# Kernel optimization log

Measured on AMD Instinct MI355X. Metric: run time of the kernel, lower is better.

## Reference

```python
import jax, jax.numpy as jnp
import numpy as np

B, N, D = 8, 1024, 768
H = 12
HD = D // H  # 64
SCALE = HD ** -0.5


def setup_inputs() -> dict:
    key = jax.random.key(0)
    k1, k2, k3 = jax.random.split(key, 3)
    x = jax.random.normal(k1, (B, N, D), dtype=jnp.float32)
    qkv_w = jax.random.normal(k2, (3 * D, D), dtype=jnp.float32) * 0.02
    proj_w = jax.random.normal(k3, (D, D), dtype=jnp.float32) * 0.02
    proj_b = jnp.zeros((D,), dtype=jnp.float32)
    return {"x": x, "qkv_w": qkv_w, "proj_w": proj_w, "proj_b": proj_b}


def reference(x, qkv_w, proj_w, proj_b):
    # qkv projection: [B,N,3D] -> [3,B,H,N,HD]
    qkv = jnp.einsum('bnd,ed->bne', x, qkv_w)
    qkv = qkv.reshape(B, N, 3, H, HD).transpose(2, 0, 3, 1, 4)
    q, k, v = qkv[0], qkv[1], qkv[2]
    # scaled dot-product attention
    attn = jnp.einsum('bhqd,bhkd->bhqk', q * SCALE, k)
    attn = jax.nn.softmax(attn, axis=-1)
    out = jnp.einsum('bhqk,bhkd->bhqd', attn, v)
    out = out.transpose(0, 2, 1, 3).reshape(B, N, D)
    # output projection
    return jnp.einsum('bnd,ed->bne', out, proj_w) + proj_b
```

## Files before the change

### kernel.cpp

```cpp
#include <hip/hip_runtime.h>

typedef unsigned short ushort;
typedef __attribute__((ext_vector_type(4)))  float  f32x4;
typedef __attribute__((ext_vector_type(16))) float  f32x16;
typedef __attribute__((ext_vector_type(8)))  short  s16x8;
typedef __attribute__((ext_vector_type(4)))  ushort u16x4;
typedef __attribute__((ext_vector_type(4)))  unsigned u32x4;

#define MFMA16(a, b, c) __builtin_amdgcn_mfma_f32_16x16x32_bf16((a), (b), (c), 0, 0, 0)
#define MFMA32(a, b, c) __builtin_amdgcn_mfma_f32_32x32x16_bf16((a), (b), (c), 0, 0, 0)

__device__ __forceinline__ ushort f2bf(float f) {
    unsigned u = __builtin_bit_cast(unsigned, f);
    u = (u + 0x7FFF + ((u >> 16) & 1)) >> 16;
    return (ushort)u;
}

__device__ __forceinline__ unsigned cvtpk_bf16(float lo, float hi) {
    unsigned r;
    asm("v_cvt_pk_bf16_f32 %0, %1, %2" : "=v"(r) : "v"(lo), "v"(hi));
    return r;
}
__device__ __forceinline__ void plswap(unsigned& a, unsigned& b) {
    asm volatile("v_permlane32_swap_b32 %0, %1" : "+v"(a), "+v"(b));
}
__device__ __forceinline__ float pairmax(float x) {
    return fmaxf(x, __shfl_xor(x, 32));
}
__device__ __forceinline__ float pairsum(float x) {
    return x + __shfl_xor(x, 32);
}
__device__ __forceinline__ float fast_exp2(float x) {
    float r;
    asm("v_exp_f32 %0, %1" : "=v"(r) : "v"(x));
    return r;
}

__device__ __forceinline__ void gload_lds16(const ushort* g, ushort* l) {
    __builtin_amdgcn_global_load_lds(
        (const __attribute__((address_space(1))) void*)g,
        (__attribute__((address_space(3))) void*)l, 16, 0, 0);
}

__global__ __launch_bounds__(256) void cvt_f32_bf16(
    const float* __restrict__ in, ushort* __restrict__ out, int n4)
{
    int i = blockIdx.x * blockDim.x + threadIdx.x;
    const int stride = gridDim.x * blockDim.x;
    for (; i < n4; i += stride) {
        const float4 v = ((const float4*)in)[i];
        u16x4 o;
        o[0] = f2bf(v.x); o[1] = f2bf(v.y); o[2] = f2bf(v.z); o[3] = f2bf(v.w);
        ((u16x4*)out)[i] = o;
    }
}

__device__ __forceinline__ void gemm128_mainloop(
    const ushort* __restrict__ A, const ushort* __restrict__ B, int K,
    int row0, int col0, ushort* As, ushort* Bs, f32x4 acc[4][4])
{
    const int t  = threadIdx.x;
    const int l  = t & 63;
    const int w  = t >> 6;
    const int lr = l & 15, lg = l >> 4;
    const int wm = w >> 1, wn = w & 1;

#pragma unroll
    for (int m = 0; m < 4; m++)
#pragma unroll
        for (int n = 0; n < 4; n++) acc[m][n] = (f32x4){0.f, 0.f, 0.f, 0.f};

    const ushort* ga0 = A + (row0 + (t >> 2)) * K + (t & 3) * 8;
    const ushort* gb0 = B + (col0 + (t >> 2)) * K + (t & 3) * 8;
    const int rowsz = 64 * K;
    ushort* la0 = As + t * 8;
    ushort* lb0 = Bs + t * 8;

    auto STAGE = [&](int kt, int buf) {
        const int k0  = kt * 32;
        const int off = buf * 4096;
        gload_lds16(ga0 + k0,         la0 + off);
        gload_lds16(ga0 + rowsz + k0, la0 + off + 2048);
        gload_lds16(gb0 + k0,         lb0 + off);
        gload_lds16(gb0 + rowsz + k0, lb0 + off + 2048);
    };
    auto COMPUTE = [&](int buf) {
        const ushort* Ab = As + buf * 4096;
        const ushort* Bb = Bs + buf * 4096;
        s16x8 af[4], bfr[4];
#pragma unroll
        for (int m = 0; m < 4; m++)
            af[m] = *(const s16x8*)&Ab[(wm * 64 + m * 16 + lr) * 32 + lg * 8];
#pragma unroll
        for (int n = 0; n < 4; n++)
            bfr[n] = *(const s16x8*)&Bb[(wn * 64 + n * 16 + lr) * 32 + lg * 8];
        __builtin_amdgcn_s_setprio(1);
#pragma unroll
        for (int m = 0; m < 4; m++)
#pragma unroll
            for (int n = 0; n < 4; n++)
                acc[m][n] = MFMA16(af[m], bfr[n], acc[m][n]);
        __builtin_amdgcn_s_setprio(0);
    };

    const int nt = K >> 5;
    STAGE(0, 0);
    STAGE(1, 1);
    asm volatile("s_waitcnt vmcnt(4)" ::: "memory");
    __builtin_amdgcn_s_barrier();

#define GSTEP(IT, CBUF, SBUF)                                          \
    {                                                                  \
        const int sk = (IT) + 2;                                       \
        const bool st = sk < nt;                                       \
        if (st) STAGE(sk, SBUF);                                       \
        COMPUTE(CBUF);                                                 \
        if (st) { asm volatile("s_waitcnt vmcnt(4)" ::: "memory"); }   \
        else    { asm volatile("s_waitcnt vmcnt(0)" ::: "memory"); }   \
        __builtin_amdgcn_s_barrier();                                  \
    }

    for (int base = 0; base < nt; base += 3) {
        GSTEP(base,     0, 2);
        GSTEP(base + 1, 1, 0);
        GSTEP(base + 2, 2, 1);
    }
#undef GSTEP
}

__global__ __launch_bounds__(256) void qkv_gemm(
    const ushort* __restrict__ X, const ushort* __restrict__ W,
    ushort* __restrict__ qb, ushort* __restrict__ kb, ushort* __restrict__ vb)
{
    __shared__ __align__(16) ushort As[3 * 128 * 32];
    __shared__ __align__(16) ushort Bs[3 * 128 * 32];
    f32x4 acc[4][4];
    const int br = blockIdx.x, bc = blockIdx.y;
    gemm128_mainloop(X, W, 768, br * 128, bc * 128, As, Bs, acc);

    const int t = threadIdx.x, l = t & 63, w = t >> 6;
    const int lr = l & 15, lg = l >> 4, wm = w >> 1, wn = w & 1;
    const int p = (bc * 128) / 768;
    const int mrow0 = br * 128 + wm * 64 + lg * 4;
    const int ecolB = bc * 128 + wn * 64 + lr;
    const float QSCALE = 0.125f * 1.44269504088896f;

#pragma unroll
    for (int n = 0; n < 4; n++) {
        const int e   = ecolB + n * 16;
        const int rem = e - p * 768;
        const int h   = rem >> 6;
        const int hd  = rem & 63;
#pragma unroll
        for (int m = 0; m < 4; m++) {
            const int mr = mrow0 + m * 16;
            const int b  = mr >> 10;
            const int nn = mr & 1023;
            const f32x4 v = acc[m][n];
            const int bh = b * 12 + h;
            if (p == 0) {
                ushort* dst = qb + (bh * 1024 + nn) * 64 + hd;
#pragma unroll
                for (int r = 0; r < 4; r++) dst[r * 64] = f2bf(v[r] * QSCALE);
            } else if (p == 1) {
                ushort* dst = kb + (bh * 1024 + nn) * 64 + hd;
#pragma unroll
                for (int r = 0; r < 4; r++) dst[r * 64] = f2bf(v[r]);
            } else {
                u16x4 pk;
                pk[0] = f2bf(v[0]); pk[1] = f2bf(v[1]);
                pk[2] = f2bf(v[2]); pk[3] = f2bf(v[3]);
                *(u16x4*)(vb + (bh * 64 + hd) * 1024 + nn) = pk;
            }
        }
    }
}

__global__ __launch_bounds__(256) void attn_kernel(
    const ushort* __restrict__ qb, const ushort* __restrict__ kb,
    const ushort* __restrict__ vb, ushort* __restrict__ ao)
{
    __shared__ __align__(16) ushort KV[2][4096];
    const int bh = blockIdx.x, qt = blockIdx.y;
    const int b = bh / 12, h = bh - b * 12;
    const int t = threadIdx.x, l = t & 63, w = t >> 6;
    const int lq = l & 31, hi = l >> 5;
    const int qr0 = qt * 128 + w * 32;

    const int l3 = l >> 3, l7 = l & 7;
    const int ku = w * 8 + l3;
    const int pfv = l7 ^ l3;
    const char* ksrc = (const char*)kb + (size_t)(bh * 1024 + ku) * 128
                     + ((l7 ^ l3) << 4);
    const char* vsrc = (const char*)vb + (size_t)(bh * 64 + ku + 32 * ((pfv >> 2) & 1)) * 2048
                     + ((pfv & 3) << 4);
    ushort* kdst = &KV[0][0]    + w * 512 + l * 8;
    ushort* vdst = &KV[0][2048] + w * 512 + l * 8;

    const ushort* qlane = qb + (bh * 1024 + qr0 + lq) * 64 + hi * 8;
    s16x8 qf[4];
#pragma unroll
    for (int s = 0; s < 4; s++) qf[s] = *(const s16x8*)(qlane + s * 16);

    float m = -__builtin_inff();
    float lsum = 0.f;
    f32x16 o0 = {}, o1 = {};

    gload_lds16((const ushort*)ksrc, kdst);
    gload_lds16((const ushort*)vsrc, vdst);
    __syncthreads();

    const int fx = (lq & 7) << 4;
    for (int it = 0; it < 32; ++it) {
        const int cur = it & 1;
        if (it < 31) {
            const int kvn = (it + 1) * 32;
            gload_lds16((const ushort*)(ksrc + kvn * 128), kdst + (cur ^ 1) * 4096);
            gload_lds16((const ushort*)(vsrc + kvn * 2),   vdst + (cur ^ 1) * 4096);
        }
        const char* Kb = (const char*)&KV[cur][0];
        const char* Vb = (const char*)&KV[cur][2048];

        s16x8 kf[4];
#pragma unroll
        for (int s = 0; s < 4; s++)
            kf[s] = *(const s16x8*)(Kb + lq * 128 + ((hi * 16 + s * 32) ^ fx));

        f32x16 sa = {};
        __builtin_amdgcn_s_setprio(1);
#pragma unroll
        for (int s = 0; s < 4; s++) sa = MFMA32(kf[s], qf[s], sa);
        __builtin_amdgcn_s_setprio(0);

        float tm[8];
#pragma unroll
        for (int r = 0; r < 8; r++) tm[r] = fmaxf(sa[r], sa[r + 8]);
#pragma unroll
        for (int s = 4; s; s >>= 1)
#pragma unroll
            for (int r = 0; r < s; r++) tm[r] = fmaxf(tm[r], tm[r + s]);
        const float mx = pairmax(tm[0]);

        if (!__all(mx <= m + 8.f)) {
            const float mn = fmaxf(m, mx);
            const float fac = fast_exp2(m - mn);
            m = mn;
            lsum *= fac;
#pragma unroll
            for (int r = 0; r < 16; r++) { o0[r] *= fac; o1[r] *= fac; }
        }

        float p[16];
#pragma unroll
        for (int r = 0; r < 16; r++) p[r] = fast_exp2(sa[r] - m);
        float ts[8];
#pragma unroll
        for (int r = 0; r < 8; r++) ts[r] = p[r] + p[r + 8];
#pragma unroll
        for (int s = 4; s; s >>= 1)
#pragma unroll
            for (int r = 0; r < s; r++) ts[r] += ts[r + s];
        lsum += pairsum(ts[0]);

        s16x8 pfr[2];
#pragma unroll
        for (int slot = 0; slot < 2; slot++) {
            const int r0 = slot * 8;
            unsigned a0 = cvtpk_bf16(p[r0 + 0], p[r0 + 1]);
            unsigned a1 = cvtpk_bf16(p[r0 + 4], p[r0 + 5]);
            plswap(a0, a1);
            unsigned b0 = cvtpk_bf16(p[r0 + 2], p[r0 + 3]);
            unsigned b1 = cvtpk_bf16(p[r0 + 6], p[r0 + 7]);
            plswap(b0, b1);
            const u32x4 u = {a0, b0, a1, b1};
            pfr[slot] = __builtin_bit_cast(s16x8, u);
        }

        s16x8 vf[2][2];
#pragma unroll
        for (int half = 0; half < 2; half++)
#pragma unroll
            for (int s = 0; s < 2; s++)
                vf[half][s] = *(const s16x8*)(Vb + lq * 128 + ((half * 64 + hi * 16 + s * 32) ^ fx));
        __builtin_amdgcn_s_setprio(1);
        o0 = MFMA32(vf[0][0], pfr[0], o0);
        o1 = MFMA32(vf[1][0], pfr[0], o1);
        o0 = MFMA32(vf[0][1], pfr[1], o0);
        o1 = MFMA32(vf[1][1], pfr[1], o1);
        __builtin_amdgcn_s_setprio(0);

        __syncthreads();
    }

    const float inv = 1.f / lsum;
    ushort* op = ao + (b * 1024 + qr0 + lq) * 768 + h * 64 + 4 * hi;
#pragma unroll
    for (int i = 0; i < 4; i++) {
        u16x4 pk0, pk1;
#pragma unroll
        for (int j = 0; j < 4; j++) {
            pk0[j] = f2bf(o0[4 * i + j] * inv);
            pk1[j] = f2bf(o1[4 * i + j] * inv);
        }
        *(u16x4*)(op + 8 * i)      = pk0;
        *(u16x4*)(op + 32 + 8 * i) = pk1;
    }
}

__global__ __launch_bounds__(256) void proj_gemm(
    const ushort* __restrict__ A, const ushort* __restrict__ W,
    const float* __restrict__ bias, float* __restrict__ out)
{
    __shared__ __align__(16) ushort As[3 * 128 * 32];
    __shared__ __align__(16) ushort Bs[3 * 128 * 32];
    f32x4 acc[4][4];
    const int br = blockIdx.x, bc = blockIdx.y;
    gemm128_mainloop(A, W, 768, br * 128, bc * 128, As, Bs, acc);

    const int t = threadIdx.x, l = t & 63, w = t >> 6;
    const int lr = l & 15, lg = l >> 4, wm = w >> 1, wn = w & 1;
    const int mrow0 = br * 128 + wm * 64 + lg * 4;
    const int ecolB = bc * 128 + wn * 64 + lr;

#pragma unroll
    for (int n = 0; n < 4; n++) {
        const int e = ecolB + n * 16;
        const float bv = bias[e];
#pragma unroll
        for (int m = 0; m < 4; m++) {
            const int mr = mrow0 + m * 16;
#pragma unroll
            for (int r = 0; r < 4; r++)
                out[(mr + r) * 768 + e] = acc[m][n][r] + bv;
        }
    }
}

extern "C" void kernel_launch(void* const* d_in, const int* in_sizes, int n_in,
                              void* d_out, int out_size, void* d_ws, size_t ws_size,
                              hipStream_t stream)
{
    const float* x  = (const float*)d_in[0];
    const float* wq = (const float*)d_in[1];
    const float* wp = (const float*)d_in[2];
    const float* pb = (const float*)d_in[3];
    float* out = (float*)d_out;

    const int NX = 8 * 1024 * 768;
    const int NQ = 2304 * 768;
    const int NP = 768 * 768;
    const int SEG = 8 * 12 * 1024 * 64;

    ushort* xb  = (ushort*)d_ws;
    ushort* wqb = xb + NX;
    ushort* wpb = wqb + NQ;
    ushort* qb  = wpb + NP;
    ushort* kb  = qb + SEG;
    ushort* vb  = kb + SEG;
    ushort* ao  = xb;

    cvt_f32_bf16<<<2048, 256, 0, stream>>>(x,  xb,  NX / 4);
    cvt_f32_bf16<<<1024, 256, 0, stream>>>(wq, wqb, NQ / 4);
    cvt_f32_bf16<<<576,  256, 0, stream>>>(wp, wpb, NP / 4);

    qkv_gemm  <<<dim3(64, 18), 256, 0, stream>>>(xb, wqb, qb, kb, vb);
    attn_kernel<<<dim3(96, 8), 256, 0, stream>>>(qb, kb, vb, ao);
    proj_gemm <<<dim3(64, 6),  256, 0, stream>>>(ao, wpb, pb, out);
}
```

Before: 120.8 us.

## Widen GEMM tiles to 128x256, swizzle LDS, and fuse conversion kernels

```diff
diff --git a/kernel.cpp b/kernel.cpp
--- a/kernel.cpp
+++ b/kernel.cpp
@@ -42,22 +42,28 @@
         (__attribute__((address_space(3))) void*)l, 16, 0, 0);
 }
 
-__global__ __launch_bounds__(256) void cvt_f32_bf16(
-    const float* __restrict__ in, ushort* __restrict__ out, int n4)
+__global__ __launch_bounds__(256) void cvt_all(
+    const float* __restrict__ x, const float* __restrict__ wq,
+    const float* __restrict__ wp, ushort* __restrict__ out,
+    int n4x, int n4q, int n4p)
 {
     int i = blockIdx.x * blockDim.x + threadIdx.x;
     const int stride = gridDim.x * blockDim.x;
-    for (; i < n4; i += stride) {
-        const float4 v = ((const float4*)in)[i];
+    const int total = n4x + n4q + n4p;
+    for (; i < total; i += stride) {
+        float4 v;
+        if (i < n4x)            v = ((const float4*)x)[i];
+        else if (i < n4x + n4q) v = ((const float4*)wq)[i - n4x];
+        else                    v = ((const float4*)wp)[i - n4x - n4q];
         u16x4 o;
         o[0] = f2bf(v.x); o[1] = f2bf(v.y); o[2] = f2bf(v.z); o[3] = f2bf(v.w);
         ((u16x4*)out)[i] = o;
     }
 }
 
-__device__ __forceinline__ void gemm128_mainloop(
+__device__ __forceinline__ void gemm_mainloop(
     const ushort* __restrict__ A, const ushort* __restrict__ B, int K,
-    int row0, int col0, ushort* As, ushort* Bs, f32x4 acc[4][4])
+    int row0, int col0, ushort* As, ushort* Bs, f32x4 acc[4][8])
 {
     const int t  = threadIdx.x;
     const int l  = t & 63;
@@ -68,45 +74,50 @@
 #pragma unroll
     for (int m = 0; m < 4; m++)
 #pragma unroll
-        for (int n = 0; n < 4; n++) acc[m][n] = (f32x4){0.f, 0.f, 0.f, 0.f};
-
-    const ushort* ga0 = A + (row0 + (t >> 2)) * K + (t & 3) * 8;
-    const ushort* gb0 = B + (col0 + (t >> 2)) * K + (t & 3) * 8;
+        for (int n = 0; n < 8; n++) acc[m][n] = (f32x4){0.f, 0.f, 0.f, 0.f};
+
+    const int slot = (t & 3) ^ ((t >> 3) & 3);
+    const ushort* ga0 = A + (row0 + (t >> 2)) * K + slot * 8;
+    const ushort* gb0 = B + (col0 + (t >> 2)) * K + slot * 8;
     const int rowsz = 64 * K;
     ushort* la0 = As + t * 8;
     ushort* lb0 = Bs + t * 8;
 
     auto STAGE = [&](int kt, int buf) {
-        const int k0  = kt * 32;
-        const int off = buf * 4096;
-        gload_lds16(ga0 + k0,         la0 + off);
-        gload_lds16(ga0 + rowsz + k0, la0 + off + 2048);
-        gload_lds16(gb0 + k0,         lb0 + off);
-        gload_lds16(gb0 + rowsz + k0, lb0 + off + 2048);
+        const int k0 = kt * 32;
+        ushort* la = la0 + buf * 4096;
+        ushort* lb = lb0 + buf * 8192;
+        gload_lds16(ga0 + k0,             la);
+        gload_lds16(ga0 + rowsz + k0,     la + 2048);
+        gload_lds16(gb0 + k0,             lb);
+        gload_lds16(gb0 + rowsz + k0,     lb + 2048);
+        gload_lds16(gb0 + 2 * rowsz + k0, lb + 4096);
+        gload_lds16(gb0 + 3 * rowsz + k0, lb + 6144);
     };
+    const int sx = (lg ^ ((lr >> 1) & 3)) * 8;
     auto COMPUTE = [&](int buf) {
         const ushort* Ab = As + buf * 4096;
-        const ushort* Bb = Bs + buf * 4096;
-        s16x8 af[4], bfr[4];
+        const ushort* Bb = Bs + buf * 8192;
+        s16x8 af[4], bf[8];
 #pragma unroll
         for (int m = 0; m < 4; m++)
-            af[m] = *(const s16x8*)&Ab[(wm * 64 + m * 16 + lr) * 32 + lg * 8];
-#pragma unroll
-        for (int n = 0; n < 4; n++)
-            bfr[n] = *(const s16x8*)&Bb[(wn * 64 + n * 16 + lr) * 32 + lg * 8];
+            af[m] = *(const s16x8*)&Ab[(wm * 64 + m * 16 + lr) * 32 + sx];
+#pragma unroll
+        for (int n = 0; n < 8; n++)
+            bf[n] = *(const s16x8*)&Bb[(wn * 128 + n * 16 + lr) * 32 + sx];
         __builtin_amdgcn_s_setprio(1);
 #pragma unroll
         for (int m = 0; m < 4; m++)
 #pragma unroll
-            for (int n = 0; n < 4; n++)
-                acc[m][n] = MFMA16(af[m], bfr[n], acc[m][n]);
+            for (int n = 0; n < 8; n++)
+                acc[m][n] = MFMA16(af[m], bf[n], acc[m][n]);
         __builtin_amdgcn_s_setprio(0);
     };
 
     const int nt = K >> 5;
     STAGE(0, 0);
     STAGE(1, 1);
-    asm volatile("s_waitcnt vmcnt(4)" ::: "memory");
+    asm volatile("s_waitcnt vmcnt(6)" ::: "memory");
     __builtin_amdgcn_s_barrier();
 
 #define GSTEP(IT, CBUF, SBUF)                                          \
@@ -115,7 +126,7 @@
         const bool st = sk < nt;                                       \
         if (st) STAGE(sk, SBUF);                                       \
         COMPUTE(CBUF);                                                 \
-        if (st) { asm volatile("s_waitcnt vmcnt(4)" ::: "memory"); }   \
+        if (st) { asm volatile("s_waitcnt vmcnt(6)" ::: "memory"); }   \
         else    { asm volatile("s_waitcnt vmcnt(0)" ::: "memory"); }   \
         __builtin_amdgcn_s_barrier();                                  \
     }
@@ -128,25 +139,25 @@
 #undef GSTEP
 }
 
-__global__ __launch_bounds__(256) void qkv_gemm(
+__global__ __launch_bounds__(256, 2) void qkv_gemm(
     const ushort* __restrict__ X, const ushort* __restrict__ W,
     ushort* __restrict__ qb, ushort* __restrict__ kb, ushort* __restrict__ vb)
 {
     __shared__ __align__(16) ushort As[3 * 128 * 32];
-    __shared__ __align__(16) ushort Bs[3 * 128 * 32];
-    f32x4 acc[4][4];
+    __shared__ __align__(16) ushort Bs[3 * 256 * 32];
+    f32x4 acc[4][8];
     const int br = blockIdx.x, bc = blockIdx.y;
-    gemm128_mainloop(X, W, 768, br * 128, bc * 128, As, Bs, acc);
+    gemm_mainloop(X, W, 768, br * 128, bc * 256, As, Bs, acc);
 
     const int t = threadIdx.x, l = t & 63, w = t >> 6;
     const int lr = l & 15, lg = l >> 4, wm = w >> 1, wn = w & 1;
-    const int p = (bc * 128) / 768;
+    const int p = (bc * 256) / 768;
     const int mrow0 = br * 128 + wm * 64 + lg * 4;
-    const int ecolB = bc * 128 + wn * 64 + lr;
+    const int ecolB = bc * 256 + wn * 128 + lr;
     const float QSCALE = 0.125f * 1.44269504088896f;
 
 #pragma unroll
-    for (int n = 0; n < 4; n++) {
+    for (int n = 0; n < 8; n++) {
         const int e   = ecolB + n * 16;
         const int rem = e - p * 768;
         const int h   = rem >> 6;
@@ -307,23 +318,23 @@
     }
 }
 
-__global__ __launch_bounds__(256) void proj_gemm(
+__global__ __launch_bounds__(256, 2) void proj_gemm(
     const ushort* __restrict__ A, const ushort* __restrict__ W,
     const float* __restrict__ bias, float* __restrict__ out)
 {
     __shared__ __align__(16) ushort As[3 * 128 * 32];
-    __shared__ __align__(16) ushort Bs[3 * 128 * 32];
-    f32x4 acc[4][4];
+    __shared__ __align__(16) ushort Bs[3 * 256 * 32];
+    f32x4 acc[4][8];
     const int br = blockIdx.x, bc = blockIdx.y;
-    gemm128_mainloop(A, W, 768, br * 128, bc * 128, As, Bs, acc);
+    gemm_mainloop(A, W, 768, br * 128, bc * 256, As, Bs, acc);
 
     const int t = threadIdx.x, l = t & 63, w = t >> 6;
     const int lr = l & 15, lg = l >> 4, wm = w >> 1, wn = w & 1;
     const int mrow0 = br * 128 + wm * 64 + lg * 4;
-    const int ecolB = bc * 128 + wn * 64 + lr;
-
-#pragma unroll
-    for (int n = 0; n < 4; n++) {
+    const int ecolB = bc * 256 + wn * 128 + lr;
+
+#pragma unroll
+    for (int n = 0; n < 8; n++) {
         const int e = ecolB + n * 16;
         const float bv = bias[e];
 #pragma unroll
@@ -359,11 +370,9 @@
     ushort* vb  = kb + SEG;
     ushort* ao  = xb;
 
-    cvt_f32_bf16<<<2048, 256, 0, stream>>>(x,  xb,  NX / 4);
-    cvt_f32_bf16<<<1024, 256, 0, stream>>>(wq, wqb, NQ / 4);
-    cvt_f32_bf16<<<576,  256, 0, stream>>>(wp, wpb, NP / 4);
-
-    qkv_gemm  <<<dim3(64, 18), 256, 0, stream>>>(xb, wqb, qb, kb, vb);
+    cvt_all<<<2048, 256, 0, stream>>>(x, wq, wp, xb, NX / 4, NQ / 4, NP / 4);
+
+    qkv_gemm  <<<dim3(64, 9), 256, 0, stream>>>(xb, wqb, qb, kb, vb);
     attn_kernel<<<dim3(96, 8), 256, 0, stream>>>(qb, kb, vb, ao);
-    proj_gemm <<<dim3(64, 6),  256, 0, stream>>>(ao, wpb, pb, out);
-}
+    proj_gemm <<<dim3(64, 3), 256, 0, stream>>>(ao, wpb, pb, out);
+}
```

New measurement: 148.7 us. 23.1% more time.
